# Kernel tuning notes

Hardware: AMD Instinct MI355X
Metric: run time of the kernel (lower is better)

## Reference

```python
import jax, jax.numpy as jnp
import numpy as np

V_ORIG = 32000   # original embedding vocab
V_NEW = 8000     # reparameterized vocab (size of down/up stacks and index_mapping)
D = 1024         # embedding dim
R = 16           # low-rank dim
N = 16384        # number of indices looked up


def setup_inputs() -> dict:
    key = jax.random.key(0)
    k1, k2, k3, k4, k5 = jax.random.split(key, 5)
    indices = jax.random.randint(k1, (N,), 0, V_NEW, dtype=jnp.int64)
    # index_mapping: dict new_index -> original_index, materialized as a lookup array
    index_map = jax.random.randint(k2, (V_NEW,), 0, V_ORIG, dtype=jnp.int64)
    emb_weight = jax.random.normal(k3, (V_ORIG, D), dtype=jnp.float32) * 0.02
    down = jax.random.normal(k4, (V_NEW, D, R), dtype=jnp.float32) * (1.0 / np.sqrt(D))
    up = jax.random.normal(k5, (V_NEW, R, D), dtype=jnp.float32) * (1.0 / np.sqrt(R))
    return {"indices": indices, "index_map": index_map,
            "emb_weight": emb_weight, "down": down, "up": up}


def reference(indices, index_map, emb_weight, down, up):
    # Gather original embeddings via the index mapping: [N, D]
    e = emb_weight[index_map[indices]]
    # Per-index low-rank projection: ([1,D] @ [D,R]) @ [R,D], batched over N
    h = jnp.einsum('nd,ndr->nr', e, down[indices])        # [N, R]
    out = jnp.einsum('nr,nrd->nd', h, up[indices])        # [N, D]
    # Original stacks per-index [1, D] results -> [N, 1, D]
    return out[:, None, :]
```

## Files before the change

### kernel.cpp

```cpp
#include <hip/hip_runtime.h>
#include <hip/hip_bf16.h>


#define DDIM 1024
#define RDIM 16

__global__ __launch_bounds__(256) void init_head_kernel(int* __restrict__ head, int V) {
    int v = blockIdx.x * 256 + threadIdx.x;
    if (v < V) head[v] = -1;
}

__global__ __launch_bounds__(256) void link_kernel(const int* __restrict__ idx,
                                                   int* __restrict__ head,
                                                   int* __restrict__ next, int n) {
    int i = blockIdx.x * 256 + threadIdx.x;
    if (i < n) next[i] = atomicExch(&head[idx[i]], i);
}

__global__ __launch_bounds__(256) void rows_ll_kernel(
    const int* __restrict__ index_map,
    const float* __restrict__ emb,
    const float* __restrict__ down,
    const float* __restrict__ up,
    const int* __restrict__ head,
    const int* __restrict__ next,
    float* __restrict__ out)
{
    const int v = blockIdx.x;
    int n0 = head[v];
    if (n0 < 0) return;

    const int tid  = threadIdx.x;
    const float* __restrict__ e  = emb  + (size_t)index_map[v] * DDIM;
    const float* __restrict__ dn = down + (size_t)v * (DDIM * RDIM);
    const float* __restrict__ u  = up   + (size_t)v * (RDIM * DDIM);

    const int rq   = (tid & 3) * 4;
    const int dgrp = tid >> 2;

    float4 dq[16];
    float  ev[16];
    #pragma unroll
    for (int k = 0; k < 16; ++k) {
        const int d = dgrp + (k << 6);
        dq[k] = *(const float4*)(dn + (size_t)d * RDIM + rq);
        ev[k] = e[d];
    }
    float4 uvec[RDIM];
    #pragma unroll
    for (int r = 0; r < RDIM; ++r)
        uvec[r] = *(const float4*)(u + (size_t)r * DDIM + tid * 4);

    float4 hp = make_float4(0.f, 0.f, 0.f, 0.f);
    #pragma unroll
    for (int k = 0; k < 16; ++k) {
        hp.x += ev[k] * dq[k].x;
        hp.y += ev[k] * dq[k].y;
        hp.z += ev[k] * dq[k].z;
        hp.w += ev[k] * dq[k].w;
    }
    #pragma unroll
    for (int m = 4; m < 64; m <<= 1) {
        hp.x += __shfl_xor(hp.x, m, 64);
        hp.y += __shfl_xor(hp.y, m, 64);
        hp.z += __shfl_xor(hp.z, m, 64);
        hp.w += __shfl_xor(hp.w, m, 64);
    }
    __shared__ float hs[4][RDIM];
    const int lane = tid & 63, wid = tid >> 6;
    if (lane < 4) {
        hs[wid][rq + 0] = hp.x;
        hs[wid][rq + 1] = hp.y;
        hs[wid][rq + 2] = hp.z;
        hs[wid][rq + 3] = hp.w;
    }
    __syncthreads();
    float hf[RDIM];
    #pragma unroll
    for (int r = 0; r < RDIM; ++r)
        hf[r] = hs[0][r] + hs[1][r] + hs[2][r] + hs[3][r];

    float4 acc = make_float4(0.f, 0.f, 0.f, 0.f);
    #pragma unroll
    for (int r = 0; r < RDIM; ++r) {
        acc.x += hf[r] * uvec[r].x;
        acc.y += hf[r] * uvec[r].y;
        acc.z += hf[r] * uvec[r].z;
        acc.w += hf[r] * uvec[r].w;
    }

    int n = n0;
    while (n >= 0) {
        *(float4*)(out + (size_t)n * DDIM + tid * 4) = acc;
        n = next[n];
    }
}

__global__ __launch_bounds__(256) void rows_direct_kernel(
    const int* __restrict__ indices,
    const int* __restrict__ index_map,
    const float* __restrict__ emb,
    const float* __restrict__ down,
    const float* __restrict__ up,
    float* __restrict__ out)
{
    const int nn  = blockIdx.x;
    const int v   = indices[nn];
    const int tid = threadIdx.x;
    const float* __restrict__ e  = emb  + (size_t)index_map[v] * DDIM;
    const float* __restrict__ dn = down + (size_t)v * (DDIM * RDIM);
    const float* __restrict__ u  = up   + (size_t)v * (RDIM * DDIM);

    const int rq   = (tid & 3) * 4;
    const int dgrp = tid >> 2;
    float4 dq[16];
    float  ev[16];
    #pragma unroll
    for (int k = 0; k < 16; ++k) {
        const int d = dgrp + (k << 6);
        dq[k] = *(const float4*)(dn + (size_t)d * RDIM + rq);
        ev[k] = e[d];
    }
    float4 uvec[RDIM];
    #pragma unroll
    for (int r = 0; r < RDIM; ++r)
        uvec[r] = *(const float4*)(u + (size_t)r * DDIM + tid * 4);

    float4 hp = make_float4(0.f, 0.f, 0.f, 0.f);
    #pragma unroll
    for (int k = 0; k < 16; ++k) {
        hp.x += ev[k] * dq[k].x; hp.y += ev[k] * dq[k].y;
        hp.z += ev[k] * dq[k].z; hp.w += ev[k] * dq[k].w;
    }
    #pragma unroll
    for (int m = 4; m < 64; m <<= 1) {
        hp.x += __shfl_xor(hp.x, m, 64);
        hp.y += __shfl_xor(hp.y, m, 64);
        hp.z += __shfl_xor(hp.z, m, 64);
        hp.w += __shfl_xor(hp.w, m, 64);
    }
    __shared__ float hs[4][RDIM];
    const int lane = tid & 63, wid = tid >> 6;
    if (lane < 4) {
        hs[wid][rq + 0] = hp.x; hs[wid][rq + 1] = hp.y;
        hs[wid][rq + 2] = hp.z; hs[wid][rq + 3] = hp.w;
    }
    __syncthreads();
    float hf[RDIM];
    #pragma unroll
    for (int r = 0; r < RDIM; ++r)
        hf[r] = hs[0][r] + hs[1][r] + hs[2][r] + hs[3][r];

    float4 acc = make_float4(0.f, 0.f, 0.f, 0.f);
    #pragma unroll
    for (int r = 0; r < RDIM; ++r) {
        acc.x += hf[r] * uvec[r].x; acc.y += hf[r] * uvec[r].y;
        acc.z += hf[r] * uvec[r].z; acc.w += hf[r] * uvec[r].w;
    }
    *(float4*)(out + (size_t)nn * DDIM + tid * 4) = acc;
}

extern "C" void kernel_launch(void* const* d_in, const int* in_sizes, int n_in,
                              void* d_out, int out_size, void* d_ws, size_t ws_size,
                              hipStream_t stream)
{
    const int*   indices   = (const int*)d_in[0];
    const int*   index_map = (const int*)d_in[1];
    const float* emb       = (const float*)d_in[2];
    const float* down      = (const float*)d_in[3];
    const float* up        = (const float*)d_in[4];
    float*       out       = (float*)d_out;

    const int N = in_sizes[0];
    const int V = in_sizes[1];

    const size_t ws_need = (size_t)(V + N) * sizeof(int);

    if (ws_size >= ws_need) {
        int* head = (int*)d_ws;
        int* next = head + V;
        init_head_kernel<<<(V + 255) / 256, 256, 0, stream>>>(head, V);
        link_kernel<<<(N + 255) / 256, 256, 0, stream>>>(indices, head, next, N);
        rows_ll_kernel<<<V, 256, 0, stream>>>(index_map, emb, down, up, head, next, out);
    } else {
        rows_direct_kernel<<<N, 256, 0, stream>>>(indices, index_map, emb, down, up, out);
    }
}
```

Before: 214.6 us.

## Map one wavefront per vocab row instead of one block per row

Each 64-lane wavefront now handles a whole vocab row, so four rows share a 256-thread block. The shared-memory reduction and __syncthreads are removed, and the final h vector is redistributed across lanes with xor shuffles and selects. This cuts block-level synchronization and launch granularity, but each wave now streams all of down and up for its row in a loop, which raises per-wave serial work and register pressure. It also lowers the number of loads in flight per row.

```diff
diff --git a/kernel.cpp b/kernel.cpp
--- a/kernel.cpp
+++ b/kernel.cpp
@@ -17,48 +17,49 @@
     if (i < n) next[i] = atomicExch(&head[idx[i]], i);
 }
 
-__global__ __launch_bounds__(256) void rows_ll_kernel(
+static __device__ __forceinline__ float4 sel4(bool c, float4 a, float4 b) {
+    float4 r;
+    r.x = c ? a.x : b.x;
+    r.y = c ? a.y : b.y;
+    r.z = c ? a.z : b.z;
+    r.w = c ? a.w : b.w;
+    return r;
+}
+
+__global__ __launch_bounds__(256) void fused_wave_kernel(
     const int* __restrict__ index_map,
     const float* __restrict__ emb,
     const float* __restrict__ down,
     const float* __restrict__ up,
     const int* __restrict__ head,
     const int* __restrict__ next,
-    float* __restrict__ out)
+    float* __restrict__ out, int V)
 {
-    const int v = blockIdx.x;
-    int n0 = head[v];
+    const int lane = threadIdx.x & 63;
+    const int v    = (blockIdx.x << 2) | (threadIdx.x >> 6);
+    if (v >= V) return;
+    const int n0 = head[v];
     if (n0 < 0) return;
 
-    const int tid  = threadIdx.x;
     const float* __restrict__ e  = emb  + (size_t)index_map[v] * DDIM;
     const float* __restrict__ dn = down + (size_t)v * (DDIM * RDIM);
     const float* __restrict__ u  = up   + (size_t)v * (RDIM * DDIM);
 
-    const int rq   = (tid & 3) * 4;
-    const int dgrp = tid >> 2;
-
-    float4 dq[16];
-    float  ev[16];
-    #pragma unroll
-    for (int k = 0; k < 16; ++k) {
-        const int d = dgrp + (k << 6);
-        dq[k] = *(const float4*)(dn + (size_t)d * RDIM + rq);
-        ev[k] = e[d];
-    }
-    float4 uvec[RDIM];
-    #pragma unroll
-    for (int r = 0; r < RDIM; ++r)
-        uvec[r] = *(const float4*)(u + (size_t)r * DDIM + tid * 4);
+    const int c0   = lane & 3;
+    const int dgrp = lane >> 2;
 
     float4 hp = make_float4(0.f, 0.f, 0.f, 0.f);
-    #pragma unroll
-    for (int k = 0; k < 16; ++k) {
-        hp.x += ev[k] * dq[k].x;
-        hp.y += ev[k] * dq[k].y;
-        hp.z += ev[k] * dq[k].z;
-        hp.w += ev[k] * dq[k].w;
-    }
+    #pragma unroll 8
+    for (int k = 0; k < 64; ++k) {
+        const int d = dgrp + (k << 4);
+        const float ed = e[d];
+        const float4 dq = *(const float4*)(dn + (size_t)d * RDIM + (c0 << 2));
+        hp.x += ed * dq.x;
+        hp.y += ed * dq.y;
+        hp.z += ed * dq.z;
+        hp.w += ed * dq.w;
+    }
+
     #pragma unroll
     for (int m = 4; m < 64; m <<= 1) {
         hp.x += __shfl_xor(hp.x, m, 64);
@@ -66,32 +67,57 @@
         hp.z += __shfl_xor(hp.z, m, 64);
         hp.w += __shfl_xor(hp.w, m, 64);
     }
-    __shared__ float hs[4][RDIM];
-    const int lane = tid & 63, wid = tid >> 6;
-    if (lane < 4) {
-        hs[wid][rq + 0] = hp.x;
-        hs[wid][rq + 1] = hp.y;
-        hs[wid][rq + 2] = hp.z;
-        hs[wid][rq + 3] = hp.w;
-    }
-    __syncthreads();
-    float hf[RDIM];
-    #pragma unroll
-    for (int r = 0; r < RDIM; ++r)
-        hf[r] = hs[0][r] + hs[1][r] + hs[2][r] + hs[3][r];
-
-    float4 acc = make_float4(0.f, 0.f, 0.f, 0.f);
-    #pragma unroll
-    for (int r = 0; r < RDIM; ++r) {
-        acc.x += hf[r] * uvec[r].x;
-        acc.y += hf[r] * uvec[r].y;
-        acc.z += hf[r] * uvec[r].z;
-        acc.w += hf[r] * uvec[r].w;
+
+    float4 t1;
+    t1.x = __shfl_xor(hp.x, 1, 64);
+    t1.y = __shfl_xor(hp.y, 1, 64);
+    t1.z = __shfl_xor(hp.z, 1, 64);
+    t1.w = __shfl_xor(hp.w, 1, 64);
+    const bool odd = (c0 & 1) != 0;
+    float4 pe = sel4(odd, t1, hp);
+    float4 po = sel4(odd, hp, t1);
+    float4 pe2, po2;
+    pe2.x = __shfl_xor(pe.x, 2, 64);
+    pe2.y = __shfl_xor(pe.y, 2, 64);
+    pe2.z = __shfl_xor(pe.z, 2, 64);
+    pe2.w = __shfl_xor(pe.w, 2, 64);
+    po2.x = __shfl_xor(po.x, 2, 64);
+    po2.y = __shfl_xor(po.y, 2, 64);
+    po2.z = __shfl_xor(po.z, 2, 64);
+    po2.w = __shfl_xor(po.w, 2, 64);
+    const bool hi = (c0 & 2) != 0;
+    const float4 q0 = sel4(hi, pe2, pe);
+    const float4 q2 = sel4(hi, pe, pe2);
+    const float4 q1 = sel4(hi, po2, po);
+    const float4 q3 = sel4(hi, po, po2);
+
+    float4 a0 = make_float4(0.f, 0.f, 0.f, 0.f);
+    float4 a1 = a0, a2 = a0, a3 = a0;
+    #pragma unroll
+    for (int j = 0; j < 4; ++j) {
+        const float4 qj = (j == 0) ? q0 : (j == 1) ? q1 : (j == 2) ? q2 : q3;
+        #pragma unroll
+        for (int t = 0; t < 4; ++t) {
+            const float hf = (t == 0) ? qj.x : (t == 1) ? qj.y : (t == 2) ? qj.z : qj.w;
+            const float* __restrict__ ur = u + (size_t)(j * 4 + t) * DDIM + (lane << 2);
+            const float4 u0 = *(const float4*)(ur + 0);
+            const float4 u1 = *(const float4*)(ur + 256);
+            const float4 u2 = *(const float4*)(ur + 512);
+            const float4 u3 = *(const float4*)(ur + 768);
+            a0.x += hf * u0.x; a0.y += hf * u0.y; a0.z += hf * u0.z; a0.w += hf * u0.w;
+            a1.x += hf * u1.x; a1.y += hf * u1.y; a1.z += hf * u1.z; a1.w += hf * u1.w;
+            a2.x += hf * u2.x; a2.y += hf * u2.y; a2.z += hf * u2.z; a2.w += hf * u2.w;
+            a3.x += hf * u3.x; a3.y += hf * u3.y; a3.z += hf * u3.z; a3.w += hf * u3.w;
+        }
     }
 
     int n = n0;
     while (n >= 0) {
-        *(float4*)(out + (size_t)n * DDIM + tid * 4) = acc;
+        float* o = out + (size_t)n * DDIM + (lane << 2);
+        *(float4*)(o + 0)   = a0;
+        *(float4*)(o + 256) = a1;
+        *(float4*)(o + 512) = a2;
+        *(float4*)(o + 768) = a3;
         n = next[n];
     }
 }
@@ -102,35 +128,27 @@
     const float* __restrict__ emb,
     const float* __restrict__ down,
     const float* __restrict__ up,
-    float* __restrict__ out)
+    float* __restrict__ out, int N)
 {
-    const int nn  = blockIdx.x;
-    const int v   = indices[nn];
-    const int tid = threadIdx.x;
+    const int lane = threadIdx.x & 63;
+    const int nn   = (blockIdx.x << 2) | (threadIdx.x >> 6);
+    if (nn >= N) return;
+    const int v = indices[nn];
+
     const float* __restrict__ e  = emb  + (size_t)index_map[v] * DDIM;
     const float* __restrict__ dn = down + (size_t)v * (DDIM * RDIM);
     const float* __restrict__ u  = up   + (size_t)v * (RDIM * DDIM);
 
-    const int rq   = (tid & 3) * 4;
-    const int dgrp = tid >> 2;
-    float4 dq[16];
-    float  ev[16];
-    #pragma unroll
-    for (int k = 0; k < 16; ++k) {
-        const int d = dgrp + (k << 6);
-        dq[k] = *(const float4*)(dn + (size_t)d * RDIM + rq);
-        ev[k] = e[d];
-    }
-    float4 uvec[RDIM];
-    #pragma unroll
-    for (int r = 0; r < RDIM; ++r)
-        uvec[r] = *(const float4*)(u + (size_t)r * DDIM + tid * 4);
+    const int c0   = lane & 3;
+    const int dgrp = lane >> 2;
 
     float4 hp = make_float4(0.f, 0.f, 0.f, 0.f);
-    #pragma unroll
-    for (int k = 0; k < 16; ++k) {
-        hp.x += ev[k] * dq[k].x; hp.y += ev[k] * dq[k].y;
-        hp.z += ev[k] * dq[k].z; hp.w += ev[k] * dq[k].w;
+    #pragma unroll 8
+    for (int k = 0; k < 64; ++k) {
+        const int d = dgrp + (k << 4);
+        const float ed = e[d];
+        const float4 dq = *(const float4*)(dn + (size_t)d * RDIM + (c0 << 2));
+        hp.x += ed * dq.x; hp.y += ed * dq.y; hp.z += ed * dq.z; hp.w += ed * dq.w;
     }
     #pragma unroll
     for (int m = 4; m < 64; m <<= 1) {
@@ -139,25 +157,53 @@
         hp.z += __shfl_xor(hp.z, m, 64);
         hp.w += __shfl_xor(hp.w, m, 64);
     }
-    __shared__ float hs[4][RDIM];
-    const int lane = tid & 63, wid = tid >> 6;
-    if (lane < 4) {
-        hs[wid][rq + 0] = hp.x; hs[wid][rq + 1] = hp.y;
-        hs[wid][rq + 2] = hp.z; hs[wid][rq + 3] = hp.w;
-    }
-    __syncthreads();
-    float hf[RDIM];
-    #pragma unroll
-    for (int r = 0; r < RDIM; ++r)
-        hf[r] = hs[0][r] + hs[1][r] + hs[2][r] + hs[3][r];
-
-    float4 acc = make_float4(0.f, 0.f, 0.f, 0.f);
-    #pragma unroll
-    for (int r = 0; r < RDIM; ++r) {
-        acc.x += hf[r] * uvec[r].x; acc.y += hf[r] * uvec[r].y;
-        acc.z += hf[r] * uvec[r].z; acc.w += hf[r] * uvec[r].w;
-    }
-    *(float4*)(out + (size_t)nn * DDIM + tid * 4) = acc;
+    float4 t1;
+    t1.x = __shfl_xor(hp.x, 1, 64);
+    t1.y = __shfl_xor(hp.y, 1, 64);
+    t1.z = __shfl_xor(hp.z, 1, 64);
+    t1.w = __shfl_xor(hp.w, 1, 64);
+    const bool odd = (c0 & 1) != 0;
+    float4 pe = sel4(odd, t1, hp);
+    float4 po = sel4(odd, hp, t1);
+    float4 pe2, po2;
+    pe2.x = __shfl_xor(pe.x, 2, 64);
+    pe2.y = __shfl_xor(pe.y, 2, 64);
+    pe2.z = __shfl_xor(pe.z, 2, 64);
+    pe2.w = __shfl_xor(pe.w, 2, 64);
+    po2.x = __shfl_xor(po.x, 2, 64);
+    po2.y = __shfl_xor(po.y, 2, 64);
+    po2.z = __shfl_xor(po.z, 2, 64);
+    po2.w = __shfl_xor(po.w, 2, 64);
+    const bool hi = (c0 & 2) != 0;
+    const float4 q0 = sel4(hi, pe2, pe);
+    const float4 q2 = sel4(hi, pe, pe2);
+    const float4 q1 = sel4(hi, po2, po);
+    const float4 q3 = sel4(hi, po, po2);
+
+    float4 a0 = make_float4(0.f, 0.f, 0.f, 0.f);
+    float4 a1 = a0, a2 = a0, a3 = a0;
+    #pragma unroll
+    for (int j = 0; j < 4; ++j) {
+        const float4 qj = (j == 0) ? q0 : (j == 1) ? q1 : (j == 2) ? q2 : q3;
+        #pragma unroll
+        for (int t = 0; t < 4; ++t) {
+            const float hf = (t == 0) ? qj.x : (t == 1) ? qj.y : (t == 2) ? qj.z : qj.w;
+            const float* __restrict__ ur = u + (size_t)(j * 4 + t) * DDIM + (lane << 2);
+            const float4 u0 = *(const float4*)(ur + 0);
+            const float4 u1 = *(const float4*)(ur + 256);
+            const float4 u2 = *(const float4*)(ur + 512);
+            const float4 u3 = *(const float4*)(ur + 768);
+            a0.x += hf * u0.x; a0.y += hf * u0.y; a0.z += hf * u0.z; a0.w += hf * u0.w;
+            a1.x += hf * u1.x; a1.y += hf * u1.y; a1.z += hf * u1.z; a1.w += hf * u1.w;
+            a2.x += hf * u2.x; a2.y += hf * u2.y; a2.z += hf * u2.z; a2.w += hf * u2.w;
+            a3.x += hf * u3.x; a3.y += hf * u3.y; a3.z += hf * u3.z; a3.w += hf * u3.w;
+        }
+    }
+    float* o = out + (size_t)nn * DDIM + (lane << 2);
+    *(float4*)(o + 0)   = a0;
+    *(float4*)(o + 256) = a1;
+    *(float4*)(o + 512) = a2;
+    *(float4*)(o + 768) = a3;
 }
 
 extern "C" void kernel_launch(void* const* d_in, const int* in_sizes, int n_in,
@@ -181,8 +227,10 @@
         int* next = head + V;
         init_head_kernel<<<(V + 255) / 256, 256, 0, stream>>>(head, V);
         link_kernel<<<(N + 255) / 256, 256, 0, stream>>>(indices, head, next, N);
-        rows_ll_kernel<<<V, 256, 0, stream>>>(index_map, emb, down, up, head, next, out);
+        fused_wave_kernel<<<(V + 3) / 4, 256, 0, stream>>>(index_map, emb, down, up,
+                                                           head, next, out, V);
     } else {
-        rows_direct_kernel<<<N, 256, 0, stream>>>(indices, index_map, emb, down, up, out);
-    }
-}
+        rows_direct_kernel<<<(N + 3) / 4, 256, 0, stream>>>(indices, index_map, emb,
+                                                            down, up, out, N);
+    }
+}
```

Result: no change. 217.7 us (+1.4%).
